# Kernel tuning notes

Hardware: AMD Instinct MI355X
Metric: run time of the kernel (lower is better)

The kernel has to match this reference:

```python
import jax, jax.numpy as jnp
import numpy as np

N = 100000      # nodes
E = 640000      # total edges across all relations
D_IN = 128
D_OUT = 128
R = 8           # num_rel
B = 4           # num_bases


def setup_inputs() -> dict:
    key = jax.random.key(0)
    ks = jax.random.split(key, 7)
    return {
        "X": jax.random.normal(ks[0], (N, D_IN), dtype=jnp.float32),
        "edge_src": jax.random.randint(ks[1], (E,), 0, N, dtype=jnp.int32),
        "edge_dst": jax.random.randint(ks[2], (E,), 0, N, dtype=jnp.int32),
        "edge_rel": jax.random.randint(ks[3], (E,), 0, R, dtype=jnp.int32),
        "edge_val": jax.random.uniform(ks[4], (E,), dtype=jnp.float32),
        "w_bases": jax.random.normal(ks[5], (B, D_IN, D_OUT), dtype=jnp.float32) * 0.05,
        "w_rel": jax.random.normal(ks[6], (R, B), dtype=jnp.float32) * 0.5,
    }


def reference(X, edge_src, edge_dst, edge_rel, edge_val, w_bases, w_rel):
    # Per-relation SpMM: support_r = A_r @ X, where A_r rows are destinations.
    # Fuse all relations into one gather + one segmented scatter-add.
    msg = X[edge_src] * edge_val[:, None]                      # [E, D_IN]
    seg = edge_rel.astype(jnp.int32) * N + edge_dst            # combined (rel, dst) id
    supports = jax.ops.segment_sum(msg, seg, num_segments=R * N)
    supports = supports.reshape(R, N, D_IN)                    # == concat of per-rel supports
    # Basis-decomposed relation weights: w[r] = sum_b w_rel[r,b] * w_bases[b]
    w = jnp.einsum("rb,bio->rio", w_rel, w_bases)              # [R, D_IN, D_OUT]
    # cat(supports, dim=1) @ w.view(R*D_IN, D_OUT) == sum_r supports_r @ w_r
    out = jnp.einsum("rni,rio->no", supports, w)               # [N, D_OUT]
    return out
```

## Files before the change

kernel.cpp:

```cpp
#include <hip/hip_runtime.h>
#include <stdint.h>

#define D_IN 128
#define D_OUT 128
#define NREL 8
#define NBASE 4

typedef __attribute__((ext_vector_type(8))) short short8;
typedef __attribute__((ext_vector_type(4))) float floatx4;
typedef __attribute__((ext_vector_type(2))) float floatx2;

__device__ __forceinline__ unsigned short f2bf(float f) {
  unsigned int u = __float_as_uint(f);
  u += 0x7fffu + ((u >> 16) & 1u);
  return (unsigned short)(u >> 16);
}
__device__ __forceinline__ unsigned pack2bf(float lo, float hi) {
  return (unsigned)f2bf(lo) | ((unsigned)f2bf(hi) << 16);
}
__device__ __forceinline__ float bflo(unsigned int u) { return __uint_as_float(u << 16); }
__device__ __forceinline__ float bfhi(unsigned int u) { return __uint_as_float(u & 0xffff0000u); }

__global__ void k_prep(const float4* __restrict__ X, ushort4* __restrict__ Xb, int n4,
                       const float* __restrict__ w_bases, unsigned short* __restrict__ W2T,
                       const int* __restrict__ edst, int* __restrict__ counts, int E) {
  int i = blockIdx.x * blockDim.x + threadIdx.x;
  if (i < n4) {
    float4 v = X[i];
    ushort4 o;
    o.x = f2bf(v.x); o.y = f2bf(v.y); o.z = f2bf(v.z); o.w = f2bf(v.w);
    Xb[i] = o;
  }
  if (i < 128 * 512) {
    int o = i >> 9, c = i & 511;
    int k = c >> 2, b = c & 3;
    W2T[i] = f2bf(w_bases[(b * D_IN + k) * D_OUT + o]);
  }
  if (i < E) atomicAdd(&counts[edst[i]], 1);
}

__global__ void k_scan1(const int* __restrict__ counts, int* __restrict__ localsc,
                        int* __restrict__ bsum, int Nn) {
  __shared__ int s[256];
  int i = blockIdx.x * 256 + threadIdx.x;
  int v = (i < Nn) ? counts[i] : 0;
  s[threadIdx.x] = v;
  __syncthreads();
  for (int off = 1; off < 256; off <<= 1) {
    int t = 0;
    if (threadIdx.x >= off) t = s[threadIdx.x - off];
    __syncthreads();
    s[threadIdx.x] += t;
    __syncthreads();
  }
  if (i < Nn) localsc[i] = s[threadIdx.x] - v;
  if (threadIdx.x == 255) bsum[blockIdx.x] = s[255];
}

__global__ void k_scan23(const int* __restrict__ localsc, const int* __restrict__ bsum,
                         int* __restrict__ offsets, int* __restrict__ cursor, int Nn, int E) {
  __shared__ int red[256];
  int acc = 0;
  for (int j = threadIdx.x; j < blockIdx.x; j += 256) acc += bsum[j];
  red[threadIdx.x] = acc;
  __syncthreads();
  for (int off = 128; off > 0; off >>= 1) {
    if (threadIdx.x < off) red[threadIdx.x] += red[threadIdx.x + off];
    __syncthreads();
  }
  int pref = red[0];
  int i = blockIdx.x * 256 + threadIdx.x;
  if (i < Nn) {
    int v = localsc[i] + pref;
    offsets[i] = v;
    cursor[i] = v;
  }
  if (i == 0) offsets[Nn] = E;
}

__global__ void k_bucket(const int* __restrict__ src, const int* __restrict__ dst,
                         const int* __restrict__ rel, const float* __restrict__ val,
                         const float* __restrict__ w_rel, int* __restrict__ cursor,
                         unsigned* __restrict__ srcs, float4* __restrict__ coef, int E) {
  int i = blockIdx.x * blockDim.x + threadIdx.x;
  if (i >= E) return;
  int d = dst[i];
  int pos = atomicAdd(&cursor[d], 1);
  float v = val[i];
  const float4 w = *(const float4*)(w_rel + rel[i] * 4);
  srcs[pos] = (unsigned)src[i];
  coef[pos] = make_float4(v * w.x, v * w.y, v * w.z, v * w.w);
}

__global__ __launch_bounds__(256, 4)
void k_agg_gemm(const unsigned* __restrict__ esrcs, const float4* __restrict__ ecoef,
                const int* __restrict__ offsets, const unsigned* __restrict__ Xb2,
                const unsigned short* __restrict__ W2T, float* __restrict__ out, int Nn) {
  __shared__ __align__(16) unsigned short aggS[32][520];

  const int wave = threadIdx.x >> 6, lane = threadIdx.x & 63;
  const int d0 = blockIdx.x * 32 + wave * 8;
  const floatx2 zf2 = {0.f, 0.f};

  int oidx = d0 + (lane < 8 ? lane : 8);
  if (oidx > Nn) oidx = Nn;
  const int offv = offsets[oidx];
  const int s0 = __builtin_amdgcn_readlane(offv, 0);
  const int e8 = __builtin_amdgcn_readlane(offv, 8);

  floatx2 a0 = zf2, a1 = zf2, a2 = zf2, a3 = zf2;
  int row = 0;
  int bnd = __builtin_amdgcn_readlane(offv, 1);

#define FLUSH()                                                      \
  do {                                                               \
    uint4 o_;                                                        \
    o_.x = pack2bf(a0.x, a1.x);                                      \
    o_.y = pack2bf(a2.x, a3.x);                                      \
    o_.z = pack2bf(a0.y, a1.y);                                      \
    o_.w = pack2bf(a2.y, a3.y);                                      \
    *(uint4*)&aggS[wave * 8 + row][lane * 8] = o_;                   \
    a0 = zf2; a1 = zf2; a2 = zf2; a3 = zf2;                          \
    ++row;                                                           \
    bnd = (row < 8) ? __builtin_amdgcn_readlane(offv, row + 1)       \
                    : 0x7fffffff;                                    \
  } while (0)

#define SSRC(S, BASE)                                                \
  do {                                                               \
    int b_ = (BASE);                                                 \
    int t0_ = b_ < ce ? b_ : ce;                                     \
    int t1_ = b_ + 1 < ce ? b_ + 1 : ce;                             \
    int t2_ = b_ + 2 < ce ? b_ + 2 : ce;                             \
    int t3_ = b_ + 3 < ce ? b_ + 3 : ce;                             \
    s##S##0 = esrcs[t0_]; s##S##1 = esrcs[t1_];                      \
    s##S##2 = esrcs[t2_]; s##S##3 = esrcs[t3_];                      \
  } while (0)

#define GATH(S)                                                      \
  do {                                                               \
    y##S##0 = Xb2[((size_t)s##S##0 << 6) + lane];                    \
    y##S##1 = Xb2[((size_t)s##S##1 << 6) + lane];                    \
    y##S##2 = Xb2[((size_t)s##S##2 << 6) + lane];                    \
    y##S##3 = Xb2[((size_t)s##S##3 << 6) + lane];                    \
  } while (0)

#define SCOEF(S, BASE)                                               \
  do {                                                               \
    int b_ = (BASE);                                                 \
    int t0_ = b_ < ce ? b_ : ce;                                     \
    int t1_ = b_ + 1 < ce ? b_ + 1 : ce;                             \
    int t2_ = b_ + 2 < ce ? b_ + 2 : ce;                             \
    int t3_ = b_ + 3 < ce ? b_ + 3 : ce;                             \
    c##S##0 = ecoef[t0_]; c##S##1 = ecoef[t1_];                      \
    c##S##2 = ecoef[t2_]; c##S##3 = ecoef[t3_];                      \
  } while (0)

#define ACCT1(EI, C, Y)                                              \
  do {                                                               \
    if ((EI) < e8) {                                                 \
      while ((EI) == bnd) FLUSH();                                   \
      floatx2 x_;                                                    \
      x_.x = bflo(Y);                                                \
      x_.y = bfhi(Y);                                                \
      a0 += (C).x * x_;                                              \
      a1 += (C).y * x_;                                              \
      a2 += (C).z * x_;                                              \
      a3 += (C).w * x_;                                              \
    }                                                                \
  } while (0)

#define ACCT4(S, EI0)                                                \
  do {                                                               \
    ACCT1((EI0), c##S##0, y##S##0);                                  \
    ACCT1((EI0) + 1, c##S##1, y##S##1);                              \
    ACCT1((EI0) + 2, c##S##2, y##S##2);                              \
    ACCT1((EI0) + 3, c##S##3, y##S##3);                              \
  } while (0)

  if (s0 < e8) {
    const int ce = e8 - 1;
    unsigned s00, s01, s02, s03, s10, s11, s12, s13, s20, s21, s22, s23;
    unsigned s30, s31, s32, s33, s40, s41, s42, s43, s50, s51, s52, s53;
    unsigned y00, y01, y02, y03, y10, y11, y12, y13, y20, y21, y22, y23;
    unsigned y30, y31, y32, y33, y40, y41, y42, y43, y50, y51, y52, y53;
    float4 c00, c01, c02, c03, c10, c11, c12, c13, c20, c21, c22, c23;
    float4 c30, c31, c32, c33, c40, c41, c42, c43, c50, c51, c52, c53;
    SSRC(0, s0); SSRC(1, s0 + 4); SSRC(2, s0 + 8); SSRC(3, s0 + 12);
    GATH(0); GATH(1); GATH(2);
    SCOEF(0, s0);
    int gi = s0;
    while (gi < e8) {
      SSRC(4, gi + 16); GATH(3); SCOEF(1, gi + 4); ACCT4(0, gi);
      SSRC(5, gi + 20); GATH(4); SCOEF(2, gi + 8); ACCT4(1, gi + 4);
      SSRC(0, gi + 24); GATH(5); SCOEF(3, gi + 12); ACCT4(2, gi + 8);
      SSRC(1, gi + 28); GATH(0); SCOEF(4, gi + 16); ACCT4(3, gi + 12);
      SSRC(2, gi + 32); GATH(1); SCOEF(5, gi + 20); ACCT4(4, gi + 16);
      SSRC(3, gi + 36); GATH(2); SCOEF(0, gi + 24); ACCT4(5, gi + 20);
      gi += 24;
    }
  }
  while (row < 8) FLUSH();

  __syncthreads();

  const int q = lane >> 4, r16 = lane & 15;
  const int wn = wave * 32;
  const floatx4 zero = {0.f, 0.f, 0.f, 0.f};
  floatx4 acc[2][2];
  acc[0][0] = zero; acc[0][1] = zero; acc[1][0] = zero; acc[1][1] = zero;

#pragma unroll 4
  for (int k0 = 0; k0 < 512; k0 += 32) {
    int ka = k0 + q * 8;
    short8 af[2], bfv[2];
    af[0] = *(const short8*)&aggS[r16][ka];
    af[1] = *(const short8*)&aggS[16 + r16][ka];
    bfv[0] = *(const short8*)(W2T + (size_t)(wn + r16) * 512 + ka);
    bfv[1] = *(const short8*)(W2T + (size_t)(wn + 16 + r16) * 512 + ka);
#pragma unroll
    for (int i = 0; i < 2; ++i)
#pragma unroll
      for (int j = 0; j < 2; ++j)
        acc[i][j] = __builtin_amdgcn_mfma_f32_16x16x32_bf16(af[i], bfv[j], acc[i][j], 0, 0, 0);
  }

#pragma unroll
  for (int i = 0; i < 2; ++i) {
#pragma unroll
    for (int j = 0; j < 2; ++j) {
#pragma unroll
      for (int p = 0; p < 4; ++p) {
        int prow = i * 16 + q * 4 + p;
        int col = wn + j * 16 + r16;
        int grow = blockIdx.x * 32 + prow;
        if (grow < Nn) out[(size_t)grow * 128 + col] = acc[i][j][p];
      }
    }
  }
}

extern "C" void kernel_launch(void* const* d_in, const int* in_sizes, int n_in,
                              void* d_out, int out_size, void* d_ws, size_t ws_size,
                              hipStream_t stream) {
  const float* X = (const float*)d_in[0];
  const int* esrc = (const int*)d_in[1];
  const int* edst = (const int*)d_in[2];
  const int* erel = (const int*)d_in[3];
  const float* eval_ = (const float*)d_in[4];
  const float* w_bases = (const float*)d_in[5];
  const float* w_rel = (const float*)d_in[6];
  const int Nn = in_sizes[0] / D_IN;
  const int E = in_sizes[1];

  char* ws = (char*)d_ws;
  size_t off = 0;
  auto alloc = [&](size_t bytes) -> char* {
    char* p = ws + off;
    off += (bytes + 255) & ~(size_t)255;
    return p;
  };
  unsigned short* Xb = (unsigned short*)alloc((size_t)Nn * D_IN * 2);
  unsigned short* W2T = (unsigned short*)alloc((size_t)128 * 512 * 2);
  int* counts = (int*)alloc((size_t)Nn * 4);
  int* cursor = (int*)alloc((size_t)Nn * 4);
  int* offsets = (int*)alloc((size_t)(Nn + 1) * 4);
  int* localsc = (int*)alloc((size_t)Nn * 4);
  int* bsum = (int*)alloc(4096);
  unsigned* srcs = (unsigned*)alloc((size_t)E * 4);
  float4* coef = (float4*)alloc((size_t)E * 16);
  (void)ws_size;

  int n4 = Nn * D_IN / 4;
  hipMemsetAsync(counts, 0, (size_t)Nn * 4, stream);
  k_prep<<<(n4 + 255) / 256, 256, 0, stream>>>((const float4*)X, (ushort4*)Xb, n4,
                                               w_bases, W2T, edst, counts, E);

  int nb = (Nn + 255) / 256;
  k_scan1<<<nb, 256, 0, stream>>>(counts, localsc, bsum, Nn);
  k_scan23<<<nb, 256, 0, stream>>>(localsc, bsum, offsets, cursor, Nn, E);
  k_bucket<<<(E + 255) / 256, 256, 0, stream>>>(esrc, edst, erel, eval_, w_rel,
                                                cursor, srcs, coef, E);

  k_agg_gemm<<<(Nn + 31) / 32, 256, 0, stream>>>(srcs, coef, offsets,
                                                 (const unsigned*)Xb, W2T,
                                                 (float*)d_out, Nn);
}
```

Baseline: 249.9 us.

## Hand-schedule gather loads with inline asm, SGPR bases and partial vmcnt waits

The gather from the bf16 feature table now uses inline global_load_dword with the row base in scalar registers and a per-lane VGPR offset. Explicit s_waitcnt vmcnt(12) plus sched barriers keep several edge groups of loads in flight. Index clamping on src and coef prefetches is removed by padding both edge arrays with 64 entries and zeroing the padded src ids. This cuts address-computation ALU work and keeps more memory requests outstanding. The cost is fragile hand-written waitcnt accounting that could read stale data if the compiler reorders other memory operations, and some edge prefetches now read past the written coefficient entries.

```diff
diff --git a/kernel.cpp b/kernel.cpp
--- a/kernel.cpp
+++ b/kernel.cpp
@@ -83,6 +83,7 @@
                          const float* __restrict__ w_rel, int* __restrict__ cursor,
                          unsigned* __restrict__ srcs, float4* __restrict__ coef, int E) {
   int i = blockIdx.x * blockDim.x + threadIdx.x;
+  if (i < 64) srcs[E + i] = 0u;
   if (i >= E) return;
   int d = dst[i];
   int pos = atomicAdd(&cursor[d], 1);
@@ -101,6 +102,8 @@
   const int wave = threadIdx.x >> 6, lane = threadIdx.x & 63;
   const int d0 = blockIdx.x * 32 + wave * 8;
   const floatx2 zf2 = {0.f, 0.f};
+  const uint64_t xbase = (uint64_t)Xb2;
+  const unsigned loff = (unsigned)lane * 4u;
 
   int oidx = d0 + (lane < 8 ? lane : 8);
   if (oidx > Nn) oidx = Nn;
@@ -129,31 +132,34 @@
 #define SSRC(S, BASE)                                                \
   do {                                                               \
     int b_ = (BASE);                                                 \
-    int t0_ = b_ < ce ? b_ : ce;                                     \
-    int t1_ = b_ + 1 < ce ? b_ + 1 : ce;                             \
-    int t2_ = b_ + 2 < ce ? b_ + 2 : ce;                             \
-    int t3_ = b_ + 3 < ce ? b_ + 3 : ce;                             \
-    s##S##0 = esrcs[t0_]; s##S##1 = esrcs[t1_];                      \
-    s##S##2 = esrcs[t2_]; s##S##3 = esrcs[t3_];                      \
+    s##S##0 = esrcs[b_];     s##S##1 = esrcs[b_ + 1];                \
+    s##S##2 = esrcs[b_ + 2]; s##S##3 = esrcs[b_ + 3];                \
+  } while (0)
+
+#define GLOAD(Y, SRCID)                                              \
+  do {                                                               \
+    uint64_t ga_ = xbase + ((uint64_t)(SRCID) << 8);                 \
+    asm volatile("global_load_dword %0, %1, %2"                      \
+                 : "=v"(Y) : "v"(loff), "s"(ga_));                   \
   } while (0)
 
 #define GATH(S)                                                      \
   do {                                                               \
-    y##S##0 = Xb2[((size_t)s##S##0 << 6) + lane];                    \
-    y##S##1 = Xb2[((size_t)s##S##1 << 6) + lane];                    \
-    y##S##2 = Xb2[((size_t)s##S##2 << 6) + lane];                    \
-    y##S##3 = Xb2[((size_t)s##S##3 << 6) + lane];                    \
+    GLOAD(y##S##0, s##S##0); GLOAD(y##S##1, s##S##1);                \
+    GLOAD(y##S##2, s##S##2); GLOAD(y##S##3, s##S##3);                \
   } while (0)
 
 #define SCOEF(S, BASE)                                               \
   do {                                                               \
     int b_ = (BASE);                                                 \
-    int t0_ = b_ < ce ? b_ : ce;                                     \
-    int t1_ = b_ + 1 < ce ? b_ + 1 : ce;                             \
-    int t2_ = b_ + 2 < ce ? b_ + 2 : ce;                             \
-    int t3_ = b_ + 3 < ce ? b_ + 3 : ce;                             \
-    c##S##0 = ecoef[t0_]; c##S##1 = ecoef[t1_];                      \
-    c##S##2 = ecoef[t2_]; c##S##3 = ecoef[t3_];                      \
+    c##S##0 = ecoef[b_];     c##S##1 = ecoef[b_ + 1];                \
+    c##S##2 = ecoef[b_ + 2]; c##S##3 = ecoef[b_ + 3];                \
+  } while (0)
+
+#define WAITG()                                                      \
+  do {                                                               \
+    asm volatile("s_waitcnt vmcnt(12)" ::: "memory");                \
+    __builtin_amdgcn_sched_barrier(0);                               \
   } while (0)
 
 #define ACCT1(EI, C, Y)                                              \
@@ -179,7 +185,6 @@
   } while (0)
 
   if (s0 < e8) {
-    const int ce = e8 - 1;
     unsigned s00, s01, s02, s03, s10, s11, s12, s13, s20, s21, s22, s23;
     unsigned s30, s31, s32, s33, s40, s41, s42, s43, s50, s51, s52, s53;
     unsigned y00, y01, y02, y03, y10, y11, y12, y13, y20, y21, y22, y23;
@@ -191,14 +196,17 @@
     SCOEF(0, s0);
     int gi = s0;
     while (gi < e8) {
-      SSRC(4, gi + 16); GATH(3); SCOEF(1, gi + 4); ACCT4(0, gi);
-      SSRC(5, gi + 20); GATH(4); SCOEF(2, gi + 8); ACCT4(1, gi + 4);
-      SSRC(0, gi + 24); GATH(5); SCOEF(3, gi + 12); ACCT4(2, gi + 8);
-      SSRC(1, gi + 28); GATH(0); SCOEF(4, gi + 16); ACCT4(3, gi + 12);
-      SSRC(2, gi + 32); GATH(1); SCOEF(5, gi + 20); ACCT4(4, gi + 16);
-      SSRC(3, gi + 36); GATH(2); SCOEF(0, gi + 24); ACCT4(5, gi + 20);
+      GATH(3); SSRC(4, gi + 16); SCOEF(1, gi + 4);  WAITG(); ACCT4(0, gi);
+      GATH(4); SSRC(5, gi + 20); SCOEF(2, gi + 8);  WAITG(); ACCT4(1, gi + 4);
+      GATH(5); SSRC(0, gi + 24); SCOEF(3, gi + 12); WAITG(); ACCT4(2, gi + 8);
+      GATH(0); SSRC(1, gi + 28); SCOEF(4, gi + 16); WAITG(); ACCT4(3, gi + 12);
+      GATH(1); SSRC(2, gi + 32); SCOEF(5, gi + 20); WAITG(); ACCT4(4, gi + 16);
+      GATH(2); SSRC(3, gi + 36); SCOEF(0, gi + 24); WAITG(); ACCT4(5, gi + 20);
       gi += 24;
     }
+    __builtin_amdgcn_sched_barrier(0);
+    asm volatile("s_waitcnt vmcnt(0) lgkmcnt(0)" ::: "memory");
+    __builtin_amdgcn_sched_barrier(0);
   }
   while (row < 8) FLUSH();
 
@@ -267,8 +275,8 @@
   int* offsets = (int*)alloc((size_t)(Nn + 1) * 4);
   int* localsc = (int*)alloc((size_t)Nn * 4);
   int* bsum = (int*)alloc(4096);
-  unsigned* srcs = (unsigned*)alloc((size_t)E * 4);
-  float4* coef = (float4*)alloc((size_t)E * 16);
+  unsigned* srcs = (unsigned*)alloc((size_t)(E + 64) * 4);
+  float4* coef = (float4*)alloc((size_t)(E + 64) * 16);
   (void)ws_size;
 
   int n4 = Nn * D_IN / 4;
```

New measurement: 267.7 us. 7.1% more time.
